# Performance work log

Measured on AMD Instinct MI355X. Metric: run time of the kernel, lower is better.

## Reference

```python
import jax, jax.numpy as jnp
import numpy as np
from jax import lax

K = 512          # num_embeddings
D = 64           # embedding_dim
BETA = 0.25      # commitment_cost


def _conv(x, w, b, stride, pad):
    y = lax.conv_general_dilated(x, w, (stride, stride), ((pad, pad), (pad, pad)),
                                 dimension_numbers=('NCHW', 'OIHW', 'NCHW'))
    return y + b[None, :, None, None]


def _convT(x, w, b, stride, k, pad):
    # transposed conv as lhs-dilated conv; w is OIHW with O=out_channels
    p = k - 1 - pad
    y = lax.conv_general_dilated(x, w, (1, 1), ((p, p), (p, p)),
                                 lhs_dilation=(stride, stride),
                                 dimension_numbers=('NCHW', 'OIHW', 'NCHW'))
    return y + b[None, :, None, None]


def setup_inputs() -> dict:
    key = jax.random.key(0)
    ks = jax.random.split(key, 16)
    s = 0.05
    inp = {
        'x':   jax.random.uniform(ks[0], (16, 3, 256, 256), jnp.float32),
        'w1':  jax.random.normal(ks[1], (128, 3, 4, 4), jnp.float32) * s,
        'b1':  jnp.zeros((128,), jnp.float32),
        'w2':  jax.random.normal(ks[2], (256, 128, 4, 4), jnp.float32) * s,
        'b2':  jnp.zeros((256,), jnp.float32),
        'w3':  jax.random.normal(ks[3], (D, 256, 3, 3), jnp.float32) * s,
        'b3':  jnp.zeros((D,), jnp.float32),
        'emb': jax.random.uniform(ks[4], (K, D), jnp.float32, -1.0 / K, 1.0 / K),
        'wt1': jax.random.normal(ks[5], (256, D, 4, 4), jnp.float32) * s,
        'bt1': jnp.zeros((256,), jnp.float32),
        'wt2': jax.random.normal(ks[6], (128, 256, 4, 4), jnp.float32) * s,
        'bt2': jnp.zeros((128,), jnp.float32),
        'w4':  jax.random.normal(ks[7], (3, 128, 3, 3), jnp.float32) * s,
        'b4':  jnp.zeros((3,), jnp.float32),
    }
    return inp


def reference(x, w1, b1, w2, b2, w3, b3, emb, wt1, bt1, wt2, bt2, w4, b4):
    # ---- encoder ----
    h = jax.nn.relu(_conv(x, w1, b1, 2, 1))    # [B,128,128,128]
    h = jax.nn.relu(_conv(h, w2, b2, 2, 1))    # [B,256,64,64]
    z = _conv(h, w3, b3, 1, 1)                 # [B,64,64,64]

    # ---- vector quantizer (faithful raw-memory reshape, as in source) ----
    flat_z = z.reshape(-1, D)                                 # [N,D]
    dists = (jnp.sum(flat_z ** 2, axis=1, keepdims=True)
             + jnp.sum(emb ** 2, axis=1)
             - 2.0 * flat_z @ emb.T)                          # [N,K]
    idx = jnp.argmin(dists, axis=1)                           # [N]
    quantized = emb[idx].reshape(z.shape)                     # gather == onehot @ emb

    e_latent = jnp.mean((lax.stop_gradient(quantized) - z) ** 2)
    q_latent = jnp.mean((quantized - lax.stop_gradient(z)) ** 2)
    vq_loss = q_latent + BETA * e_latent

    z_q = z + lax.stop_gradient(quantized - z)                # straight-through

    n = flat_z.shape[0]
    avg_probs = jnp.zeros((K,), jnp.float32).at[idx].add(1.0) / n
    perplexity = jnp.exp(-jnp.sum(avg_probs * jnp.log(avg_probs + 1e-10)))

    # ---- decoder (computed in the original forward; its output is unused) ----
    d = jax.nn.relu(_convT(z_q, wt1, bt1, 2, 4, 1))           # [B,256,128,128]
    d = jax.nn.relu(_convT(d, wt2, bt2, 2, 4, 1))             # [B,128,256,256]
    _x_recon = jax.nn.sigmoid(_conv(d, w4, b4, 1, 1))         # [B,3,256,256]

    return (z_q, vq_loss, perplexity)
```

## Files before the change

### kernel.cpp

```cpp
#include <hip/hip_runtime.h>
#include <math.h>

typedef __attribute__((ext_vector_type(8))) short bf16x8;
typedef __attribute__((ext_vector_type(4))) float f32x4;
typedef __attribute__((ext_vector_type(4))) unsigned u32x4;
typedef __attribute__((ext_vector_type(2))) unsigned u32x2;

#define H1P_OFF  0ull
#define H2P_OFF  35143680ull
#define WQ2H_OFF 53526528ull
#define WQ3H_OFF 54050816ull
#define EQ_OFF   54247424ull
#define EN_OFF   54280192ull
#define HIST_OFF 54280704ull
#define SSEP_OFF 54284800ull
#define WQ1H_OFF 54285824ull

__device__ inline unsigned short f2bf(float f) {
  unsigned u = __builtin_bit_cast(unsigned, f);
  return (unsigned short)((u + 0x7fffu + ((u >> 16) & 1u)) >> 16);
}
__device__ inline float bf2f(unsigned short h) {
  return __builtin_bit_cast(float, (unsigned)h << 16);
}
__device__ inline unsigned packsplit(float v) {
  unsigned short h = f2bf(v);
  unsigned short l = f2bf(v - bf2f(h));
  return (unsigned)h | ((unsigned)l << 16);
}
#define SEL_HI 0x05040100u
#define SEL_LO 0x07060302u
__device__ inline bf16x8 mkfrag(const u32x4 p, const u32x4 q, unsigned sel) {
  u32x4 r;
  r[0] = __builtin_amdgcn_perm(p[1], p[0], sel);
  r[1] = __builtin_amdgcn_perm(p[3], p[2], sel);
  r[2] = __builtin_amdgcn_perm(q[1], q[0], sel);
  r[3] = __builtin_amdgcn_perm(q[3], q[2], sel);
  return __builtin_bit_cast(bf16x8, r);
}

__global__ void pack_all_k(const float* __restrict__ w1, const float* __restrict__ w2,
                           const float* __restrict__ w3, const float* __restrict__ emb,
                           unsigned short* __restrict__ wh1, unsigned short* __restrict__ wh2,
                           unsigned short* __restrict__ wh3, unsigned* __restrict__ eq,
                           float* __restrict__ enorm) {
  int blk = blockIdx.x;
  if (blk < 2048) {
    int i = blk * 256 + threadIdx.x;
    int j = i & 7, l = (i >> 3) & 63, fg = (i >> 9) & 15, ks = i >> 13;
    int row = fg * 16 + (l & 15);
    int k = ks * 32 + (l >> 4) * 8 + j;
    wh2[i] = f2bf(w2[row * 2048 + k]);
  } else if (blk < 2816) {
    int i = (blk - 2048) * 256 + threadIdx.x;
    int j = i & 7, l = (i >> 3) & 63, fg = (i >> 9) & 3, ks = i >> 11;
    int row = fg * 16 + (l & 15);
    int k = ks * 32 + (l >> 4) * 8 + j;
    int ci = k / 12, rb = k - ci * 12, kh = rb >> 2, kw = rb & 3;
    wh3[i] = (kw < 3) ? f2bf(w3[((row * 256 + ci) * 3 + kh) * 3 + kw]) : (unsigned short)0;
  } else if (blk < 2848) {
    int i = (blk - 2816) * 256 + threadIdx.x;
    int j = i & 7, l = (i >> 3) & 63, fg = (i >> 9) & 7, ks = i >> 12;
    int row = fg * 16 + (l & 15);
    int k = ks * 32 + (l >> 4) * 8 + j;
    int ci = k >> 4, r = k & 15, kh = r >> 2, kw = r & 3;
    wh1[i] = (ci < 3) ? f2bf(w1[((row * 3 + ci) * 4 + kh) * 4 + kw]) : (unsigned short)0;
  } else {
    int i = (blk - 2848) * 256 + threadIdx.x;
    if (i < 32768) {
      int e = i & 3, l = (i >> 2) & 63, j = (i >> 8) & 1, fg = (i >> 9) & 31, ks = i >> 14;
      int row = fg * 16 + (l & 15);
      int d = ks * 32 + (l >> 4) * 8 + j * 4 + e;
      eq[i] = packsplit(emb[row * 64 + d]);
    }
    if (i < 512) {
      float s = 0.f;
#pragma unroll
      for (int d = 0; d < 64; ++d) { float e = emb[i * 64 + d]; s += e * e; }
      enorm[i] = s;
    }
  }
}

__global__ void halo_k(unsigned* __restrict__ h1p, unsigned* __restrict__ h2p) {
  int i = blockIdx.x * 256 + threadIdx.x;
  if (i < 2048 * 520) {
    int p = i / 520, c = i - p * 520; int r, cc;
    if (c < 132)      { r = 0;   cc = c; }
    else if (c < 264) { r = 129; cc = c - 132; }
    else if (c < 392) { r = c - 264 + 1; cc = 0; }
    else              { r = c - 392 + 1; cc = 129; }
    h1p[(size_t)p * 130 * 132 + r * 132 + cc] = 0u;
  } else {
    int j = i - 2048 * 520;
    if (j >= 4096 * 328) return;
    int p = j / 328, c = j - p * 328; int r, cc;
    if (c < 68)       { r = 0;  cc = c; }
    else if (c < 136) { r = 65; cc = c - 68; }
    else { int c2 = c - 136; int which = c2 >> 6; r = 1 + (c2 & 63);
           cc = (which == 0) ? 0 : (which == 1 ? 65 : 66); }
    h2p[(size_t)p * 66 * 68 + r * 68 + cc] = 0u;
  }
}

template <int IC, int KHW, int OC, int IHP, int IWP, int S, int NWX, int NWC,
          int YB, bool WIDE, int OSR, int OSP, int OPAD, bool SPLIT_OUT, int D, bool XSRC>
__global__ __launch_bounds__(256, 2) void convmm_k(const unsigned* __restrict__ inp,
                                                   const float* __restrict__ xsrc,
                                                   const unsigned short* __restrict__ wqh,
                                                   const float* __restrict__ bias,
                                                   unsigned* __restrict__ outp,
                                                   float* __restrict__ outf) {
  constexpr int K = IC * KHW;
  constexpr int KSUPER = K / (32 * D);
  constexpr int FGTOT = OC / 16;
  constexpr int NFRAG = OC / NWC / 16;
  constexpr int MR = 64 * NWX;
  constexpr int CELLS = (MR / 32) * D;
  constexpr int GPLANE = MR * 16;
  constexpr int HBYTES = MR * 64 * D;
  constexpr int ABYTES = MR * 128 * D;
  constexpr int LOG2NWX = (NWX == 2) ? 1 : 0;
  constexpr int LOG2MR = (NWX == 2) ? 7 : 6;

  __shared__ char smem[2 * ABYTES];

  const int tid = threadIdx.x, l = tid & 63, wv = tid >> 6;
  const int orig = (blockIdx.x & 7) * ((int)gridDim.x >> 3) + (blockIdx.x >> 3);
  const int bb = orig >> YB;
  const int y0 = orig & ((1 << YB) - 1);
  const int rsel = l & 15, gp = l >> 4;
  const int mbase = (wv & (NWX - 1)) * 64;
  const int fgbase = (wv >> LOG2NWX) * NFRAG;
  const int nbase = fgbase * 16;

  const int arow = tid & (MR - 1);
  int qs[CELLS];
  const unsigned* abase[CELLS];
#pragma unroll
  for (int c = 0; c < CELLS; ++c) {
    qs[c] = (tid >> LOG2MR) * CELLS + c;
    if constexpr (KHW == 16 && !XSRC) {
      int ci0 = qs[c] >> 2, kh = qs[c] & 3;
      abase[c] = inp + (((size_t)bb * IC + ci0) * IHP + (S * y0 + kh)) * IWP + S * arow;
    }
  }

  f32x4 acc[NFRAG][4];
#pragma unroll
  for (int nf = 0; nf < NFRAG; ++nf)
#pragma unroll
    for (int xf = 0; xf < 4; ++xf) acc[nf][xf] = (f32x4){0.f, 0.f, 0.f, 0.f};

  unsigned avA[CELLS][4], avB[CELLS][4];
  bf16x8 brA[D][NFRAG], brB[D][NFRAG];

  auto loadA = [&](int ks, unsigned (&av)[CELLS][4]) {
#pragma unroll
    for (int c = 0; c < CELLS; ++c) {
      if constexpr (XSRC) {
        int ci = (qs[c] >> 2) + 2 * D * ks;
        int kh = qs[c] & 3;
        int iy = S * y0 + kh - 1;
        bool yok = (ci < 3) && ((unsigned)iy < 256u);
        const float* xp = xsrc + ((size_t)(bb * 3 + ci) * 256 + iy) * 256;
#pragma unroll
        for (int e = 0; e < 4; ++e) {
          int ix = S * arow + e - 1;
          av[c][e] = (yok && (unsigned)ix < 256u) ? packsplit(xp[ix]) : 0u;
        }
      } else if constexpr (KHW == 16) {
        const unsigned* p = abase[c];
        av[c][0] = p[0]; av[c][1] = p[1]; av[c][2] = p[2]; av[c][3] = p[3];
        abase[c] += (size_t)(2 * D) * IHP * IWP;
      } else {
        int k = ks * (32 * D) + qs[c] * 4;
        int ci = (k * 5462) >> 16;
        int rb = k - ci * 12;
        int kh = rb >> 2;
        int yl = arow >> 6, x = arow & 63;
        const unsigned* p = inp + (((size_t)bb * IC + ci) * IHP + (y0 * 2 + yl + kh)) * IWP + x;
        av[c][0] = p[0]; av[c][1] = p[1]; av[c][2] = p[2]; av[c][3] = p[3];
      }
    }
  };
  auto writeA = [&](int buf, unsigned (&av)[CELLS][4]) {
    char* base = smem + buf * ABYTES;
#pragma unroll
    for (int cp = 0; cp < CELLS / 2; ++cp) {
      int q0 = qs[2 * cp];
      int off = (q0 >> 1) * GPLANE + (arow << 4);
      u32x4 h, lo;
      h[0]  = __builtin_amdgcn_perm(av[2 * cp][1],     av[2 * cp][0],     SEL_HI);
      h[1]  = __builtin_amdgcn_perm(av[2 * cp][3],     av[2 * cp][2],     SEL_HI);
      h[2]  = __builtin_amdgcn_perm(av[2 * cp + 1][1], av[2 * cp + 1][0], SEL_HI);
      h[3]  = __builtin_amdgcn_perm(av[2 * cp + 1][3], av[2 * cp + 1][2], SEL_HI);
      lo[0] = __builtin_amdgcn_perm(av[2 * cp][1],     av[2 * cp][0],     SEL_LO);
      lo[1] = __builtin_amdgcn_perm(av[2 * cp][3],     av[2 * cp][2],     SEL_LO);
      lo[2] = __builtin_amdgcn_perm(av[2 * cp + 1][1], av[2 * cp + 1][0], SEL_LO);
      lo[3] = __builtin_amdgcn_perm(av[2 * cp + 1][3], av[2 * cp + 1][2], SEL_LO);
      *(u32x4*)(base + off) = h;
      *(u32x4*)(base + HBYTES + off) = lo;
    }
  };
  auto loadB = [&](int ks, bf16x8 (&bh)[D][NFRAG]) {
#pragma unroll
    for (int s = 0; s < D; ++s)
#pragma unroll
      for (int nf = 0; nf < NFRAG; ++nf) {
        size_t idx = (((size_t)((ks * D + s) * FGTOT + fgbase + nf) * 64) + l) * 8;
        bh[s][nf] = *(const bf16x8*)(wqh + idx);
      }
  };
  auto step = [&](int ks, bf16x8 (&ch)[D][NFRAG], bf16x8 (&nh)[D][NFRAG],
                  unsigned (&avW)[CELLS][4], unsigned (&avL)[CELLS][4]) {
    const bool hasW = (ks + 1 < KSUPER);
    const bool hasL = (ks + 2 < KSUPER);
    if (hasW) loadB(ks + 1, nh);
    if (hasL) loadA(ks + 2, avL);
    const char* bA = smem + (ks & 1) * ABYTES;
#pragma unroll
    for (int s = 0; s < D; ++s) {
      bf16x8 ah[4], al[4];
#pragma unroll
      for (int xf = 0; xf < 4; ++xf) {
        int row = mbase + xf * 16 + rsel;
        ah[xf] = *(const bf16x8*)(bA + (s * 4 + gp) * GPLANE + (row << 4));
        al[xf] = *(const bf16x8*)(bA + HBYTES + (s * 4 + gp) * GPLANE + (row << 4));
      }
#pragma unroll
      for (int nf = 0; nf < NFRAG; ++nf) {
#pragma unroll
        for (int xf = 0; xf < 4; ++xf) {
          acc[nf][xf] = __builtin_amdgcn_mfma_f32_16x16x32_bf16(ch[s][nf], ah[xf], acc[nf][xf], 0, 0, 0);
          acc[nf][xf] = __builtin_amdgcn_mfma_f32_16x16x32_bf16(ch[s][nf], al[xf], acc[nf][xf], 0, 0, 0);
        }
      }
    }
    if (hasW) writeA((ks & 1) ^ 1, avW);
    __syncthreads();
  };

  loadB(0, brA);
  loadA(0, avA);
  writeA(0, avA);
  if (KSUPER > 1) loadA(1, avB);
  __syncthreads();

#pragma unroll 1
  for (int ks = 0; ks < KSUPER; ks += 2) {
    step(ks,     brA, brB, avB, avA);
    step(ks + 1, brB, brA, avA, avB);
  }

#pragma unroll
  for (int nf = 0; nf < NFRAG; ++nf) {
    int n0 = nbase + nf * 16 + (l >> 4) * 4;
#pragma unroll
    for (int xf = 0; xf < 4; ++xf) {
      int m = mbase + xf * 16 + rsel;
      int xo, yout;
      if constexpr (WIDE) { xo = m; yout = y0; }
      else { xo = m & 63; yout = y0 * NWX + (m >> 6); }
#pragma unroll
      for (int r = 0; r < 4; ++r) {
        float v = acc[nf][xf][r] + bias[n0 + r];
        if constexpr (SPLIT_OUT) {
          if (v < 0.f) v = 0.f;
          outp[((size_t)bb * OC + n0 + r) * OSP + (size_t)(yout + OPAD) * OSR + (xo + OPAD)] =
              packsplit(v);
        } else {
          outf[((size_t)bb * OC + n0 + r) * OSP + (size_t)yout * OSR + xo] = v;
        }
      }
    }
  }
}

__global__ __launch_bounds__(256, 2) void vqmm_k(float* __restrict__ zq,
                                                 const float* __restrict__ emb,
                                                 const unsigned* __restrict__ eq,
                                                 const float* __restrict__ enorm,
                                                 unsigned* __restrict__ hist,
                                                 float* __restrict__ ssep) {
  const int tid = threadIdx.x, l = tid & 63, wv = tid >> 6;
  float* zsrc = zq + (size_t)blockIdx.x * 4096;

  __shared__ float zf[64][64];
  __shared__ unsigned zp[4096];
  __shared__ float candd[4][64];
  __shared__ int   candi[4][64];
  __shared__ int   idxf[64];
  __shared__ unsigned hcnt[512];
  __shared__ float wsse[4];

  for (int i = tid; i < 512; i += 256) hcnt[i] = 0;

#pragma unroll
  for (int p = 0; p < 4; ++p) {
    int idx = p * 256 + tid;
    float4 v = *(const float4*)(zsrc + (size_t)idx * 4);
    int n = idx >> 4, d0 = (idx & 15) * 4;
    zf[n][d0 + 0] = v.x; zf[n][d0 + 1] = v.y;
    zf[n][d0 + 2] = v.z; zf[n][d0 + 3] = v.w;
  }
  __syncthreads();
#pragma unroll
  for (int p = 0; p < 16; ++p) {
    int idx = p * 256 + tid;
    int n = idx >> 6, d = idx & 63;
    zp[(n << 6) + ((((d >> 2) ^ (n & 15)) << 2) | (d & 3))] = packsplit(zf[n][d]);
  }
  __syncthreads();

  f32x4 acc[8][4];
#pragma unroll
  for (int nf = 0; nf < 8; ++nf)
#pragma unroll
    for (int xf = 0; xf < 4; ++xf) acc[nf][xf] = (f32x4){0.f, 0.f, 0.f, 0.f};

  const int rsel = l & 15;
#pragma unroll
  for (int ks = 0; ks < 2; ++ks) {
    bf16x8 ah[4], al[4];
    const int gk = ks * 8 + (l >> 4) * 2;
#pragma unroll
    for (int xf = 0; xf < 4; ++xf) {
      int n = xf * 16 + rsel;
      u32x4 p0 = *(const u32x4*)((const char*)zp + (n << 8) + ((gk ^ (n & 15)) << 4));
      u32x4 p1 = *(const u32x4*)((const char*)zp + (n << 8) + (((gk + 1) ^ (n & 15)) << 4));
      ah[xf] = mkfrag(p0, p1, SEL_HI);
      al[xf] = mkfrag(p0, p1, SEL_LO);
    }
#pragma unroll
    for (int nf = 0; nf < 8; ++nf) {
      int fg = wv * 8 + nf;
      u32x4 b0 = *(const u32x4*)(eq + (((size_t)((ks * 32 + fg) * 2 + 0)) << 8) + (l << 2));
      u32x4 b1 = *(const u32x4*)(eq + (((size_t)((ks * 32 + fg) * 2 + 1)) << 8) + (l << 2));
      bf16x8 wh = mkfrag(b0, b1, SEL_HI);
      bf16x8 wl = mkfrag(b0, b1, SEL_LO);
#pragma unroll
      for (int xf = 0; xf < 4; ++xf) {
        acc[nf][xf] = __builtin_amdgcn_mfma_f32_16x16x32_bf16(wh, ah[xf], acc[nf][xf], 0, 0, 0);
        acc[nf][xf] = __builtin_amdgcn_mfma_f32_16x16x32_bf16(wh, al[xf], acc[nf][xf], 0, 0, 0);
        acc[nf][xf] = __builtin_amdgcn_mfma_f32_16x16x32_bf16(wl, ah[xf], acc[nf][xf], 0, 0, 0);
      }
    }
  }

  float en[8][4];
#pragma unroll
  for (int nf = 0; nf < 8; ++nf)
#pragma unroll
    for (int r = 0; r < 4; ++r)
      en[nf][r] = enorm[wv * 128 + nf * 16 + (l >> 4) * 4 + r];

#pragma unroll
  for (int xf = 0; xf < 4; ++xf) {
    float best = 1e30f; int bidx = 0;
#pragma unroll
    for (int nf = 0; nf < 8; ++nf)
#pragma unroll
      for (int r = 0; r < 4; ++r) {
        int k = wv * 128 + nf * 16 + (l >> 4) * 4 + r;
        float dist = en[nf][r] - 2.f * acc[nf][xf][r];
        if (dist < best || (dist == best && k < bidx)) { best = dist; bidx = k; }
      }
#pragma unroll
    for (int off = 16; off <= 32; off <<= 1) {
      float ob = __shfl_xor(best, off, 64);
      int oi = __shfl_xor(bidx, off, 64);
      if (ob < best || (ob == best && oi < bidx)) { best = ob; bidx = oi; }
    }
    if (l < 16) { candd[wv][xf * 16 + l] = best; candi[wv][xf * 16 + l] = bidx; }
  }
  __syncthreads();
  if (tid < 64) {
    float best = candd[0][tid]; int bidx = candi[0][tid];
#pragma unroll
    for (int w = 1; w < 4; ++w) {
      float ob = candd[w][tid]; int oi = candi[w][tid];
      if (ob < best || (ob == best && oi < bidx)) { best = ob; bidx = oi; }
    }
    idxf[tid] = bidx;
    atomicAdd(&hcnt[bidx], 1u);
  }
  __syncthreads();

  float sse = 0.f;
#pragma unroll
  for (int p = 0; p < 16; ++p) {
    int idx = p * 256 + tid;
    int n = idx >> 6, d = idx & 63;
    float q = emb[idxf[n] * 64 + d];
    float z = zf[n][d];
    float df = q - z;
    sse += df * df;
    zsrc[idx] = q;
  }
#pragma unroll
  for (int off = 32; off > 0; off >>= 1) sse += __shfl_down(sse, off, 64);
  if (l == 0) wsse[wv] = sse;

  unsigned* hr = hist + ((blockIdx.x & 7) << 9);
  __syncthreads();
  for (int i = tid; i < 512; i += 256)
    if (hcnt[i]) atomicAdd(&hr[i], hcnt[i]);
  if (tid == 0) ssep[blockIdx.x] = wsse[0] + wsse[1] + wsse[2] + wsse[3];
}

__global__ void fin_k(const unsigned* __restrict__ hist,
                      const float* __restrict__ ssep,
                      float* __restrict__ out) {
  __shared__ float red[512];
  __shared__ float sred[512];
  int t = threadIdx.x;
  sred[t] = ssep[t] + ssep[t + 512];
  unsigned c = 0;
#pragma unroll
  for (int r = 0; r < 8; ++r) c += hist[(r << 9) + t];
  float p = (float)c * (1.f / 65536.f);
  red[t] = p * logf(p + 1e-10f);
  __syncthreads();
  for (int s = 256; s > 0; s >>= 1) {
    if (t < s) { red[t] += red[t + s]; sred[t] += sred[t + s]; }
    __syncthreads();
  }
  if (t == 0) {
    out[4194304] = 1.25f * sred[0] * (1.f / 4194304.f);
    out[4194305] = expf(-red[0]);
  }
}

extern "C" void kernel_launch(void* const* d_in, const int* in_sizes, int n_in,
                              void* d_out, int out_size, void* d_ws, size_t ws_size,
                              hipStream_t stream) {
  const float* x   = (const float*)d_in[0];
  const float* w1  = (const float*)d_in[1];
  const float* b1  = (const float*)d_in[2];
  const float* w2  = (const float*)d_in[3];
  const float* b2  = (const float*)d_in[4];
  const float* w3  = (const float*)d_in[5];
  const float* b3  = (const float*)d_in[6];
  const float* emb = (const float*)d_in[7];

  float* out = (float*)d_out;
  unsigned* wsu = (unsigned*)d_ws;
  unsigned* h1p = wsu + H1P_OFF;
  unsigned* h2p = wsu + H2P_OFF;
  unsigned short* wq1h = (unsigned short*)(wsu + WQ1H_OFF);
  unsigned short* wq2h = (unsigned short*)(wsu + WQ2H_OFF);
  unsigned short* wq3h = (unsigned short*)(wsu + WQ3H_OFF);
  unsigned* eqp = wsu + EQ_OFF;
  float* enorm = (float*)(wsu + EN_OFF);
  unsigned* hist = wsu + HIST_OFF;
  float* ssep = (float*)(wsu + SSEP_OFF);

  hipMemsetAsync(wsu + HIST_OFF, 0, 4096 * sizeof(unsigned), stream);

  pack_all_k<<<dim3(2976), dim3(256), 0, stream>>>(w1, w2, w3, emb,
                                                   wq1h, wq2h, wq3h, eqp, enorm);
  halo_k<<<dim3(9408), dim3(256), 0, stream>>>(h1p, h2p);

  convmm_k<4, 16, 128, 258, 260, 2, 2, 2, 7, true, 132, 17160, 1, true, 1, true>
      <<<dim3(2048), dim3(256), 0, stream>>>(nullptr, x, wq1h, b1, h1p, nullptr);
  convmm_k<128, 16, 256, 130, 132, 2, 1, 4, 6, false, 68, 4488, 1, true, 2, false>
      <<<dim3(1024), dim3(256), 0, stream>>>(h1p, nullptr, wq2h, b2, h2p, nullptr);
  convmm_k<256, 12, 64, 66, 68, 1, 2, 2, 5, false, 64, 4096, 0, false, 2, false>
      <<<dim3(512), dim3(256), 0, stream>>>(h2p, nullptr, wq3h, b3, nullptr, out);

  vqmm_k<<<dim3(1024), dim3(256), 0, stream>>>(out, emb, eqp, enorm, hist, ssep);
  fin_k<<<dim3(1), dim3(512), 0, stream>>>(hist, ssep, out);
}
```

Baseline: 289.2 us.

## Retile conv2 to two output rows per block with per-fragment B prefetch

Folds the halo-zeroing kernel into the weight-packing kernel, removing one launch. Conv2 is retiled from one output row with four channel-splitting waves (NWX=1, NWC=4, D=2) to two output rows with a 2x2 wave layout (NWX=2, D=1), which halves its grid. A new BDEF mode loads the weights for the next K-step one fragment at a time inside the MFMA loop and reuses a single register buffer, which lowers register pressure. The non-WIDE A-address computation is fixed so that it handles multi-row tiles. The new tiling changes per-wave data reuse and occupancy, and it leaves fewer blocks to spread across the CUs.

```diff
diff --git a/kernel.cpp b/kernel.cpp
--- a/kernel.cpp
+++ b/kernel.cpp
@@ -4,7 +4,6 @@
 typedef __attribute__((ext_vector_type(8))) short bf16x8;
 typedef __attribute__((ext_vector_type(4))) float f32x4;
 typedef __attribute__((ext_vector_type(4))) unsigned u32x4;
-typedef __attribute__((ext_vector_type(2))) unsigned u32x2;
 
 #define H1P_OFF  0ull
 #define H2P_OFF  35143680ull
@@ -43,7 +42,8 @@
                            const float* __restrict__ w3, const float* __restrict__ emb,
                            unsigned short* __restrict__ wh1, unsigned short* __restrict__ wh2,
                            unsigned short* __restrict__ wh3, unsigned* __restrict__ eq,
-                           float* __restrict__ enorm) {
+                           float* __restrict__ enorm,
+                           unsigned* __restrict__ h1p, unsigned* __restrict__ h2p) {
   int blk = blockIdx.x;
   if (blk < 2048) {
     int i = blk * 256 + threadIdx.x;
@@ -65,7 +65,7 @@
     int k = ks * 32 + (l >> 4) * 8 + j;
     int ci = k >> 4, r = k & 15, kh = r >> 2, kw = r & 3;
     wh1[i] = (ci < 3) ? f2bf(w1[((row * 3 + ci) * 4 + kh) * 4 + kw]) : (unsigned short)0;
-  } else {
+  } else if (blk < 2976) {
     int i = (blk - 2848) * 256 + threadIdx.x;
     if (i < 32768) {
       int e = i & 3, l = (i >> 2) & 63, j = (i >> 8) & 1, fg = (i >> 9) & 31, ks = i >> 14;
@@ -79,32 +79,31 @@
       for (int d = 0; d < 64; ++d) { float e = emb[i * 64 + d]; s += e * e; }
       enorm[i] = s;
     }
-  }
-}
-
-__global__ void halo_k(unsigned* __restrict__ h1p, unsigned* __restrict__ h2p) {
-  int i = blockIdx.x * 256 + threadIdx.x;
-  if (i < 2048 * 520) {
-    int p = i / 520, c = i - p * 520; int r, cc;
-    if (c < 132)      { r = 0;   cc = c; }
-    else if (c < 264) { r = 129; cc = c - 132; }
-    else if (c < 392) { r = c - 264 + 1; cc = 0; }
-    else              { r = c - 392 + 1; cc = 129; }
-    h1p[(size_t)p * 130 * 132 + r * 132 + cc] = 0u;
   } else {
-    int j = i - 2048 * 520;
-    if (j >= 4096 * 328) return;
-    int p = j / 328, c = j - p * 328; int r, cc;
-    if (c < 68)       { r = 0;  cc = c; }
-    else if (c < 136) { r = 65; cc = c - 68; }
-    else { int c2 = c - 136; int which = c2 >> 6; r = 1 + (c2 & 63);
-           cc = (which == 0) ? 0 : (which == 1 ? 65 : 66); }
-    h2p[(size_t)p * 66 * 68 + r * 68 + cc] = 0u;
+    int i = (blk - 2976) * 256 + threadIdx.x;
+    if (i < 2048 * 520) {
+      int p = i / 520, c = i - p * 520; int r, cc;
+      if (c < 132)      { r = 0;   cc = c; }
+      else if (c < 264) { r = 129; cc = c - 132; }
+      else if (c < 392) { r = c - 264 + 1; cc = 0; }
+      else              { r = c - 392 + 1; cc = 129; }
+      h1p[(size_t)p * 130 * 132 + r * 132 + cc] = 0u;
+    } else {
+      int j = i - 2048 * 520;
+      if (j >= 4096 * 328) return;
+      int p = j / 328, c = j - p * 328; int r, cc;
+      if (c < 68)       { r = 0;  cc = c; }
+      else if (c < 136) { r = 65; cc = c - 68; }
+      else { int c2 = c - 136; int which = c2 >> 6; r = 1 + (c2 & 63);
+             cc = (which == 0) ? 0 : (which == 1 ? 65 : 66); }
+      h2p[(size_t)p * 66 * 68 + r * 68 + cc] = 0u;
+    }
   }
 }
 
 template <int IC, int KHW, int OC, int IHP, int IWP, int S, int NWX, int NWC,
-          int YB, bool WIDE, int OSR, int OSP, int OPAD, bool SPLIT_OUT, int D, bool XSRC>
+          int YB, bool WIDE, int OSR, int OSP, int OPAD, bool SPLIT_OUT, int D,
+          bool XSRC, bool BDEF>
 __global__ __launch_bounds__(256, 2) void convmm_k(const unsigned* __restrict__ inp,
                                                    const float* __restrict__ xsrc,
                                                    const unsigned short* __restrict__ wqh,
@@ -142,7 +141,10 @@
     qs[c] = (tid >> LOG2MR) * CELLS + c;
     if constexpr (KHW == 16 && !XSRC) {
       int ci0 = qs[c] >> 2, kh = qs[c] & 3;
-      abase[c] = inp + (((size_t)bb * IC + ci0) * IHP + (S * y0 + kh)) * IWP + S * arow;
+      int yl = (WIDE || NWX == 1) ? 0 : (arow >> 6);
+      int xc = (WIDE || NWX == 1) ? arow : (arow & 63);
+      int ybase = WIDE ? y0 : (y0 * NWX + yl);
+      abase[c] = inp + (((size_t)bb * IC + ci0) * IHP + (S * ybase + kh)) * IWP + S * xc;
     }
   }
 
@@ -155,6 +157,10 @@
   unsigned avA[CELLS][4], avB[CELLS][4];
   bf16x8 brA[D][NFRAG], brB[D][NFRAG];
 
+  auto ldB1 = [&](int ks, int nf) -> bf16x8 {
+    size_t idx = (((size_t)(ks * FGTOT + fgbase + nf) * 64) + l) * 8;
+    return *(const bf16x8*)(wqh + idx);
+  };
   auto loadA = [&](int ks, unsigned (&av)[CELLS][4]) {
 #pragma unroll
     for (int c = 0; c < CELLS; ++c) {
@@ -207,16 +213,14 @@
 #pragma unroll
     for (int s = 0; s < D; ++s)
 #pragma unroll
-      for (int nf = 0; nf < NFRAG; ++nf) {
-        size_t idx = (((size_t)((ks * D + s) * FGTOT + fgbase + nf) * 64) + l) * 8;
-        bh[s][nf] = *(const bf16x8*)(wqh + idx);
-      }
+      for (int nf = 0; nf < NFRAG; ++nf)
+        bh[s][nf] = ldB1(ks * D + s, nf);
   };
   auto step = [&](int ks, bf16x8 (&ch)[D][NFRAG], bf16x8 (&nh)[D][NFRAG],
                   unsigned (&avW)[CELLS][4], unsigned (&avL)[CELLS][4]) {
     const bool hasW = (ks + 1 < KSUPER);
     const bool hasL = (ks + 2 < KSUPER);
-    if (hasW) loadB(ks + 1, nh);
+    if constexpr (!BDEF) { if (hasW) loadB(ks + 1, nh); }
     if (hasL) loadA(ks + 2, avL);
     const char* bA = smem + (ks & 1) * ABYTES;
 #pragma unroll
@@ -230,10 +234,17 @@
       }
 #pragma unroll
       for (int nf = 0; nf < NFRAG; ++nf) {
+        bf16x8 w;
+        if constexpr (BDEF) {
+          w = ch[s][nf];
+          if (hasW) ch[s][nf] = ldB1(ks + 1, nf);
+        } else {
+          w = ch[s][nf];
+        }
 #pragma unroll
         for (int xf = 0; xf < 4; ++xf) {
-          acc[nf][xf] = __builtin_amdgcn_mfma_f32_16x16x32_bf16(ch[s][nf], ah[xf], acc[nf][xf], 0, 0, 0);
-          acc[nf][xf] = __builtin_amdgcn_mfma_f32_16x16x32_bf16(ch[s][nf], al[xf], acc[nf][xf], 0, 0, 0);
+          acc[nf][xf] = __builtin_amdgcn_mfma_f32_16x16x32_bf16(w, ah[xf], acc[nf][xf], 0, 0, 0);
+          acc[nf][xf] = __builtin_amdgcn_mfma_f32_16x16x32_bf16(w, al[xf], acc[nf][xf], 0, 0, 0);
         }
       }
     }
@@ -250,7 +261,7 @@
 #pragma unroll 1
   for (int ks = 0; ks < KSUPER; ks += 2) {
     step(ks,     brA, brB, avB, avA);
-    step(ks + 1, brB, brA, avA, avB);
+    step(ks + 1, BDEF ? brA : brB, brA, avA, avB);
   }
 
 #pragma unroll
@@ -458,15 +469,15 @@
 
   hipMemsetAsync(wsu + HIST_OFF, 0, 4096 * sizeof(unsigned), stream);
 
-  pack_all_k<<<dim3(2976), dim3(256), 0, stream>>>(w1, w2, w3, emb,
-                                                   wq1h, wq2h, wq3h, eqp, enorm);
-  halo_k<<<dim3(9408), dim3(256), 0, stream>>>(h1p, h2p);
-
-  convmm_k<4, 16, 128, 258, 260, 2, 2, 2, 7, true, 132, 17160, 1, true, 1, true>
+  pack_all_k<<<dim3(12384), dim3(256), 0, stream>>>(w1, w2, w3, emb,
+                                                    wq1h, wq2h, wq3h, eqp, enorm,
+                                                    h1p, h2p);
+
+  convmm_k<4, 16, 128, 258, 260, 2, 2, 2, 7, true, 132, 17160, 1, true, 1, true, false>
       <<<dim3(2048), dim3(256), 0, stream>>>(nullptr, x, wq1h, b1, h1p, nullptr);
-  convmm_k<128, 16, 256, 130, 132, 2, 1, 4, 6, false, 68, 4488, 1, true, 2, false>
-      <<<dim3(1024), dim3(256), 0, stream>>>(h1p, nullptr, wq2h, b2, h2p, nullptr);
-  convmm_k<256, 12, 64, 66, 68, 1, 2, 2, 5, false, 64, 4096, 0, false, 2, false>
+  convmm_k<128, 16, 256, 130, 132, 2, 2, 2, 5, false, 68, 4488, 1, true, 1, false, true>
+      <<<dim3(512), dim3(256), 0, stream>>>(h1p, nullptr, wq2h, b2, h2p, nullptr);
+  convmm_k<256, 12, 64, 66, 68, 1, 2, 2, 5, false, 64, 4096, 0, false, 2, false, false>
       <<<dim3(512), dim3(256), 0, stream>>>(h2p, nullptr, wq3h, b3, nullptr, out);
 
   vqmm_k<<<dim3(1024), dim3(256), 0, stream>>>(out, emb, eqp, enorm, hist, ssep);
```

New measurement: 374.4 us. 29.5% more time.
